# Performance work log

Measured on AMD Instinct MI355X. Metric: run time of the kernel, lower is better.

## Reference

```python
import jax, jax.numpy as jnp
import numpy as np
import math

NB_STEPS = 50          # quadrature sub-intervals -> 51 Clenshaw-Curtis points
NUM_RNN_STEPS = 2


def _cc_weights(nb_steps):
    # Faithful port of UMNN's compute_cc_weights (Clenshaw-Curtis quadrature).
    lam = np.arange(0, nb_steps + 1).reshape(-1, 1).astype(np.float64)
    lam = np.cos((lam @ lam.T) * math.pi / nb_steps)
    lam[:, 0] = 0.5
    lam[:, -1] = 0.5 * lam[:, -1]
    lam = lam * 2.0 / nb_steps
    W = np.arange(0, nb_steps + 1).reshape(-1, 1).astype(np.float64)
    W[np.arange(1, nb_steps + 1, 2)] = 0
    W = 2.0 / (1.0 - W ** 2)
    W[0] = 1.0
    W[np.arange(1, nb_steps + 1, 2)] = 0
    cc = (lam.T @ W).astype(np.float32).reshape(-1)                      # [S]
    steps = np.cos(np.arange(0, nb_steps + 1) * math.pi / nb_steps).astype(np.float32)  # [S]
    return jnp.asarray(cc), jnp.asarray(steps)

CC_W, CC_STEPS = _cc_weights(NB_STEPS)  # S = NB_STEPS + 1 = 51


def _integrand(t, h, W1, b1, W2, b2, W3, b3, final_w):
    # IntegrandNN: MLP(cat(t,h)) -> ELU + 1 (>=0) -> fused power features -> ReLU(Linear)
    z = jnp.concatenate([t, h], axis=1)          # [N, in_d]
    z = jax.nn.relu(z @ W1.T + b1)               # [N, 128]
    z = jax.nn.relu(z @ W2.T + b2)               # [N, 128]
    z = jax.nn.elu(z @ W3.T + b3) + 1.0          # [N, 1], >= 0
    p = jnp.concatenate([z ** 1.5, z ** 2, z ** 2.5, z ** 3, z ** 3.5], axis=1)  # [N, 5]
    return jax.nn.relu((1.0 / (p + 1.0)) @ final_w.T)  # [N, 1]


def _inner_integral(x, h, params):
    # InnerUMNN: integral of IntegrandNN from x to xmax, xmax = max(x) + 10 (global scalar)
    N = x.shape[0]
    S = NB_STEPS + 1
    xmax = jnp.max(x) + 10.0
    T = x + (xmax - x) * (CC_STEPS[None, :] + 1.0) * 0.5   # [N, S]
    Tf = T.reshape(N * S, 1)
    hf = jnp.broadcast_to(h[:, None, :], (N, S, h.shape[1])).reshape(N * S, -1)
    g = _integrand(Tf, hf, *params).reshape(N, S)
    z = jnp.sum(g * CC_W[None, :], axis=1, keepdims=True)  # [N, 1]
    return z * (xmax - x) * 0.5


def _outer_integral(xT, h, params):
    # ParallelNeuralIntegral of InnerUMNN from x0 = 0 to xT; xT: [B, 1]
    B = xT.shape[0]
    S = NB_STEPS + 1
    X = xT * (CC_STEPS[None, :] + 1.0) * 0.5               # [B, S] (x0 = 0)
    Xf = X.reshape(B * S, 1)
    hf = jnp.broadcast_to(h[:, None, :], (B, S, h.shape[1])).reshape(B * S, -1)
    f = _inner_integral(Xf, hf, params).reshape(B, S)      # nested quadrature
    z = jnp.sum(f * CC_W[None, :], axis=1, keepdims=True)  # [B, 1]
    return z * xT * 0.5


def setup_inputs() -> dict:
    key = jax.random.key(0)
    ks = jax.random.split(key, 8)
    B, NF, IN_D, H = 256, 512, 64, 128
    x_ = jax.random.normal(ks[0], (B, NF), jnp.float32)
    h_ = jax.random.normal(ks[1], (B, IN_D - 1), jnp.float32)

    def lin(k, o, i):
        lim = 1.0 / np.sqrt(i)
        kw, kb = jax.random.split(k)
        return (jax.random.uniform(kw, (o, i), jnp.float32, -lim, lim),
                jax.random.uniform(kb, (o,), jnp.float32, -lim, lim))

    W1, b1 = lin(ks[2], H, IN_D)
    W2, b2 = lin(ks[3], H, H)
    W3, b3 = lin(ks[4], 1, H)
    lim5 = 1.0 / np.sqrt(5.0)
    final_w = jnp.abs(jax.random.uniform(ks[5], (1, 5), jnp.float32, -lim5, lim5))  # reset_params: abs
    log_weight = jnp.ones((1, NF), jnp.float32)            # reset_parameters: all ones
    sigmoid_param = jax.random.normal(ks[6], (1,), jnp.float32)
    return dict(x_=x_, h_=h_, W1=W1, b1=b1, W2=W2, b2=b2, W3=W3, b3=b3,
                final_w=final_w, log_weight=log_weight, sigmoid_param=sigmoid_param)


def reference(x_, h_, W1, b1, W2, b2, W3, b3, final_w, log_weight, sigmoid_param):
    params = (W1, b1, W2, b2, W3, b3, final_w)
    # compute_modular_function: F.linear then sum over dim 1 -> [B, 1]
    xm = jnp.sum(x_ @ log_weight.T, axis=1, keepdims=True)
    lam = jax.nn.sigmoid(sigmoid_param)                    # [1]
    out = jnp.zeros_like(xm)
    for _ in range(NUM_RNN_STEPS):
        xT = (1.0 - lam) * xm + lam * out
        out = _outer_integral(xT, h_, params)
    return out
```

## Files before the change

kernel.cpp:

```cpp
#include <hip/hip_runtime.h>
#include <math.h>

#define BB 256
#define NF 512
#define IND 64
#define HD 128
#define SS 51
#define NHM1 63

#define WS_LAM  0
#define WS_CCW  16
#define WS_U    80
#define WS_XM   144
#define WS_OUT1 656
#define WSH_C1  2048
#define WSH_W1  34816
#define WSH_W2F 40960

typedef _Float16 f16x8 __attribute__((ext_vector_type(8)));
typedef float    f32x16 __attribute__((ext_vector_type(16)));

__global__ void k_setup(const float* __restrict__ x_, const float* __restrict__ h_,
                        const float* __restrict__ W1, const float* __restrict__ b1,
                        const float* __restrict__ W2, const float* __restrict__ lw,
                        const float* __restrict__ sp, float* __restrict__ ws) {
    int b = blockIdx.x;
    int j = threadIdx.x;
    short* wsh = (short*)ws;

    float acc = b1[j];
    const float* w1row = W1 + j * IND;
    const float* hrow  = h_ + b * NHM1;
    #pragma unroll 7
    for (int k = 0; k < NHM1; ++k) acc = fmaf(w1row[1 + k], hrow[k], acc);
    {
        _Float16 hv = (_Float16)acc;
        short sv; __builtin_memcpy(&sv, &hv, 2);
        wsh[WSH_C1 + b * HD + j] = sv;
    }

    float s = 0.f;
    for (int k = j; k < NF; k += HD) s = fmaf(x_[b * NF + k], lw[k], s);
    __shared__ float red[HD];
    red[j] = s;
    __syncthreads();
    for (int off = 64; off > 0; off >>= 1) {
        if (j < off) red[j] += red[j + off];
        __syncthreads();
    }
    if (j == 0) ws[WS_XM + b] = red[0];

    if (b < 128) {
        int d = b * 128 + j;
        int i = d & 7, lane = (d >> 3) & 63, kn = d >> 9;
        int kk = kn >> 2, nt = kn & 3;
        int row = nt * 32 + (lane & 31);
        int k = kk * 16 + (lane >> 5) * 8 + i;
        _Float16 hv = (_Float16)W2[row * HD + k];
        short sv; __builtin_memcpy(&sv, &hv, 2);
        wsh[WSH_W2F + d] = sv;
    }

    if (b == 0) {
        if (j < SS) {
            float acc2 = 0.f;
            for (int jj = 0; jj <= 50; jj += 2) {
                float wj = (jj == 0) ? 1.f : 2.f / (1.f - (float)(jj * jj));
                float lamv;
                if (j == 0 || j == 50) {
                    lamv = 0.02f;
                } else {
                    int m = (jj * j) % 100;
                    lamv = cosf((float)m * (float)M_PI / 50.f) * 0.04f;
                }
                acc2 = fmaf(lamv, wj, acc2);
            }
            ws[WS_CCW + j] = acc2;
            float st = cosf((float)j * (float)M_PI / 50.f);
            ws[WS_U + j] = (st + 1.f) * 0.5f;
        }
        if (j == 127) ws[WS_LAM] = 1.f / (1.f + expf(-sp[0]));
    }
    if (b == 2) {
        _Float16 hv = (_Float16)W1[j * IND];
        short sv; __builtin_memcpy(&sv, &hv, 2);
        wsh[WSH_W1 + j] = sv;
    }
    if (b == 4) ws[WS_OUT1 + j] = 0.f;
    if (b == 5) ws[WS_OUT1 + 128 + j] = 0.f;
}

__launch_bounds__(256, 2)
__global__ void k_int(const float* __restrict__ b2, const float* __restrict__ W3,
                      const float* __restrict__ b3, const float* __restrict__ fw,
                      const float* __restrict__ ws, const float* __restrict__ outprev,
                      float* __restrict__ tgt, float* __restrict__ ztgt) {
    int b = blockIdx.x >> 1, half = blockIdx.x & 1;
    int tid = threadIdx.x;
    int wv = tid >> 6, l = tid & 63;
    int e32 = l & 31, h2 = l >> 5;

    __shared__ float us[SS], ccs[SS], xw[4];
    __shared__ float part[2][2][4][32];

    if (ztgt && half == 0 && tid == 0) ztgt[b] = 0.f;
    if (tid < SS) { us[tid] = ws[WS_U + tid]; ccs[tid] = ws[WS_CCW + tid]; }

    float lam = ws[WS_LAM];
    float xmv = ws[WS_XM + tid];
    float opv = outprev ? outprev[tid] : 0.f;
    float xtv = (1.f - lam) * xmv + lam * opv;
    float mx = fmaxf(xtv, 0.f);
    #pragma unroll
    for (int off = 32; off >= 1; off >>= 1) mx = fmaxf(mx, __shfl_xor(mx, off, 64));
    if (l == 0) xw[wv] = mx;
    __syncthreads();
    float xmax = fmaxf(fmaxf(xw[0], xw[1]), fmaxf(xw[2], xw[3])) + 10.f;
    float xT = (1.f - lam) * ws[WS_XM + b] + lam * (outprev ? outprev[b] : 0.f);

    const short* wsh = (const short*)ws;

    f16x8 Af[8], c1r[8], w1r[8];
    #pragma unroll
    for (int kk = 0; kk < 8; ++kk) {
        Af[kk]  = *reinterpret_cast<const f16x8*>(wsh + WSH_W2F + ((kk * 4 + wv) * 64 + l) * 8);
        c1r[kk] = *reinterpret_cast<const f16x8*>(wsh + WSH_C1 + b * HD + kk * 16 + h2 * 8);
        w1r[kk] = *reinterpret_cast<const f16x8*>(wsh + WSH_W1 + kk * 16 + h2 * 8);
    }
    float b2n[16], w3n[16];
    #pragma unroll
    for (int r = 0; r < 16; ++r) {
        int j = wv * 32 + (r & 3) + 8 * (r >> 2) + 4 * h2;
        b2n[r] = b2[j]; w3n[r] = W3[j];
    }
    float b3v = b3[0];
    float fw0 = fw[0], fw1 = fw[1], fw2 = fw[2], fw3 = fw[3], fw4 = fw[4];

    float accO = 0.f;
    int buf = 0;
    int base0 = half * 1344;

    for (int it = 0; it < 21; ++it) {
        int base = base0 + it * 64;
        float t_[2];
        #pragma unroll
        for (int ti = 0; ti < 2; ++ti) {
            int m = base + ti * 32 + e32;
            int mm = m <= 2600 ? m : 2600;
            int s  = (mm * 41121) >> 21;
            int si = mm - s * 51;
            float x = xT * us[s];
            t_[ti] = fmaf(xmax - x, us[si], x);
        }
        _Float16 th0 = (_Float16)t_[0], th1 = (_Float16)t_[1];
        f16x8 tv0 = {th0, th0, th0, th0, th0, th0, th0, th0};
        f16x8 tv1 = {th1, th1, th1, th1, th1, th1, th1, th1};
        f16x8 zf = {};

        f32x16 C0, C1;
        #pragma unroll
        for (int e = 0; e < 16; ++e) { C0[e] = 0.f; C1[e] = 0.f; }

        #pragma unroll
        for (int kk = 0; kk < 8; ++kk) {
            f16x8 B0 = __builtin_elementwise_max(__builtin_elementwise_fma(w1r[kk], tv0, c1r[kk]), zf);
            f16x8 B1 = __builtin_elementwise_max(__builtin_elementwise_fma(w1r[kk], tv1, c1r[kk]), zf);
            C0 = __builtin_amdgcn_mfma_f32_32x32x16_f16(Af[kk], B0, C0, 0, 0, 0);
            C1 = __builtin_amdgcn_mfma_f32_32x32x16_f16(Af[kk], B1, C1, 0, 0, 0);
            __builtin_amdgcn_sched_barrier(0);
        }

        {
            float s0 = 0.f;
            #pragma unroll
            for (int r = 0; r < 16; ++r) s0 = fmaf(fmaxf(C0[r] + b2n[r], 0.f), w3n[r], s0);
            s0 += __shfl_xor(s0, 32, 64);
            if (h2 == 0) part[buf][0][wv][e32] = s0;
            float s1 = 0.f;
            #pragma unroll
            for (int r = 0; r < 16; ++r) s1 = fmaf(fmaxf(C1[r] + b2n[r], 0.f), w3n[r], s1);
            s1 += __shfl_xor(s1, 32, 64);
            if (h2 == 0) part[buf][1][wv][e32] = s1;
        }
        __syncthreads();

        if (wv == 0) {
            int m = base + l;
            float zs = part[buf][h2][0][e32] + part[buf][h2][1][e32]
                     + part[buf][h2][2][e32] + part[buf][h2][3][e32] + b3v;
            float z = zs > 0.f ? zs + 1.f : __expf(zs);
            float sq = sqrtf(z);
            float p15 = z * sq, p2 = z * z, p25 = p2 * sq, p3 = p2 * z, p35 = p3 * sq;
            float g = fw0 * __builtin_amdgcn_rcpf(p15 + 1.f)
                    + fw1 * __builtin_amdgcn_rcpf(p2  + 1.f)
                    + fw2 * __builtin_amdgcn_rcpf(p25 + 1.f)
                    + fw3 * __builtin_amdgcn_rcpf(p3  + 1.f)
                    + fw4 * __builtin_amdgcn_rcpf(p35 + 1.f);
            g = fmaxf(g, 0.f);
            int valid = (m <= 2600);
            int mm = valid ? m : 2600;
            int s  = (mm * 41121) >> 21;
            int si = mm - s * 51;
            float x = xT * us[s];
            float wgt = valid ? (ccs[si] * ccs[s] * (xmax - x) * xT * 0.25f) : 0.f;
            accO = fmaf(g, wgt, accO);
        }
        buf ^= 1;
    }

    if (wv == 0) {
        #pragma unroll
        for (int off = 32; off >= 1; off >>= 1) accO += __shfl_xor(accO, off, 64);
        if (l == 0) atomicAdd(&tgt[b], accO);
    }
}

extern "C" void kernel_launch(void* const* d_in, const int* in_sizes, int n_in,
                              void* d_out, int out_size, void* d_ws, size_t ws_size,
                              hipStream_t stream) {
    (void)in_sizes; (void)n_in; (void)out_size; (void)ws_size;
    const float* x_ = (const float*)d_in[0];
    const float* h_ = (const float*)d_in[1];
    const float* W1 = (const float*)d_in[2];
    const float* b1 = (const float*)d_in[3];
    const float* W2 = (const float*)d_in[4];
    const float* b2 = (const float*)d_in[5];
    const float* W3 = (const float*)d_in[6];
    const float* b3 = (const float*)d_in[7];
    const float* fw = (const float*)d_in[8];
    const float* lw = (const float*)d_in[9];
    const float* sp = (const float*)d_in[10];
    float* wsf  = (float*)d_ws;
    float* out1 = wsf + WS_OUT1;
    float* out  = (float*)d_out;

    k_setup<<<BB, HD, 0, stream>>>(x_, h_, W1, b1, W2, lw, sp, wsf);
    k_int<<<BB * 2, 256, 0, stream>>>(b2, W3, b3, fw, wsf, nullptr, out1, out);
    k_int<<<BB * 2, 256, 0, stream>>>(b2, W3, b3, fw, wsf, out1, out, nullptr);
}
```

Before: 78.55 us.

## Precompute quadrature tables, spread epilogue across waves, defer it one iteration

Each block now builds its quadrature nodes and weights once into shared-memory tables, so the main loop no longer recomputes index decodes. The scalar epilogue (ELU, powers, reciprocals) is split across all four waves at 16 lanes each and delayed by one iteration, so it overlaps the next MFMA batch instead of serialising on wave 0. Smaller changes fold b2 into the accumulator init, split the reduction into four chains, drop the sched_barrier and use packed f16x2 FMAs. The cost is about 10.5 KB more LDS per block and a barrier placed at the end of each iteration.

```diff
diff --git a/kernel.cpp b/kernel.cpp
--- a/kernel.cpp
+++ b/kernel.cpp
@@ -17,8 +17,12 @@
 #define WSH_W1  34816
 #define WSH_W2F 40960
 
+typedef _Float16 f16x2 __attribute__((ext_vector_type(2)));
+typedef _Float16 f16x4 __attribute__((ext_vector_type(4)));
 typedef _Float16 f16x8 __attribute__((ext_vector_type(8)));
 typedef float    f32x16 __attribute__((ext_vector_type(16)));
+
+union f16x8_split { f16x8 v8; f16x2 v2[4]; };
 
 __global__ void k_setup(const float* __restrict__ x_, const float* __restrict__ h_,
                         const float* __restrict__ W1, const float* __restrict__ b1,
@@ -101,6 +105,7 @@
     int e32 = l & 31, h2 = l >> 5;
 
     __shared__ float us[SS], ccs[SS], xw[4];
+    __shared__ float t_tab[1344], wgt_tab[1344];
     __shared__ float part[2][2][4][32];
 
     if (ztgt && half == 0 && tid == 0) ztgt[b] = 0.f;
@@ -118,14 +123,38 @@
     float xmax = fmaxf(fmaxf(xw[0], xw[1]), fmaxf(xw[2], xw[3])) + 10.f;
     float xT = (1.f - lam) * ws[WS_XM + b] + lam * (outprev ? outprev[b] : 0.f);
 
+    int base0 = half * 1344;
+    #pragma unroll
+    for (int k = 0; k < 6; ++k) {
+        int idx = tid + k * 256;
+        if (idx < 1344) {
+            int m = base0 + idx;
+            int valid = (m <= 2600);
+            int mm = valid ? m : 2600;
+            int s  = (mm * 41121) >> 21;
+            int si = mm - s * 51;
+            float x = xT * us[s];
+            float range = xmax - x;
+            t_tab[idx] = fmaf(range, us[si], x);
+            wgt_tab[idx] = valid ? (ccs[si] * ccs[s] * range * xT * 0.25f) : 0.f;
+        }
+    }
+
     const short* wsh = (const short*)ws;
 
-    f16x8 Af[8], c1r[8], w1r[8];
+    f16x8 Af[8];
+    f16x2 c1p[8][4], w1p[8][4];
     #pragma unroll
     for (int kk = 0; kk < 8; ++kk) {
-        Af[kk]  = *reinterpret_cast<const f16x8*>(wsh + WSH_W2F + ((kk * 4 + wv) * 64 + l) * 8);
-        c1r[kk] = *reinterpret_cast<const f16x8*>(wsh + WSH_C1 + b * HD + kk * 16 + h2 * 8);
-        w1r[kk] = *reinterpret_cast<const f16x8*>(wsh + WSH_W1 + kk * 16 + h2 * 8);
+        Af[kk] = *reinterpret_cast<const f16x8*>(wsh + WSH_W2F + ((kk * 4 + wv) * 64 + l) * 8);
+        f16x8_split c8, w8;
+        c8.v8 = *reinterpret_cast<const f16x8*>(wsh + WSH_C1 + b * HD + kk * 16 + h2 * 8);
+        w8.v8 = *reinterpret_cast<const f16x8*>(wsh + WSH_W1 + kk * 16 + h2 * 8);
+        #pragma unroll
+        for (int p = 0; p < 4; ++p) {
+            c1p[kk][p] = c8.v2[p];
+            w1p[kk][p] = w8.v2[p];
+        }
     }
     float b2n[16], w3n[16];
     #pragma unroll
@@ -137,57 +166,71 @@
     float fw0 = fw[0], fw1 = fw[1], fw2 = fw[2], fw3 = fw[3], fw4 = fw[4];
 
     float accO = 0.f;
+    __syncthreads();
+
+    const f16x2 z2 = {(_Float16)0.f, (_Float16)0.f};
     int buf = 0;
-    int base0 = half * 1344;
 
     for (int it = 0; it < 21; ++it) {
-        int base = base0 + it * 64;
-        float t_[2];
-        #pragma unroll
-        for (int ti = 0; ti < 2; ++ti) {
-            int m = base + ti * 32 + e32;
-            int mm = m <= 2600 ? m : 2600;
-            int s  = (mm * 41121) >> 21;
-            int si = mm - s * 51;
-            float x = xT * us[s];
-            t_[ti] = fmaf(xmax - x, us[si], x);
-        }
-        _Float16 th0 = (_Float16)t_[0], th1 = (_Float16)t_[1];
-        f16x8 tv0 = {th0, th0, th0, th0, th0, th0, th0, th0};
-        f16x8 tv1 = {th1, th1, th1, th1, th1, th1, th1, th1};
-        f16x8 zf = {};
+        int base = it * 64;
+        float t0 = t_tab[base + e32];
+        float t1 = t_tab[base + 32 + e32];
+        _Float16 th0 = (_Float16)t0, th1 = (_Float16)t1;
+        f16x2 tv0 = {th0, th0};
+        f16x2 tv1 = {th1, th1};
 
         f32x16 C0, C1;
         #pragma unroll
-        for (int e = 0; e < 16; ++e) { C0[e] = 0.f; C1[e] = 0.f; }
+        for (int e = 0; e < 16; ++e) { C0[e] = b2n[e]; C1[e] = b2n[e]; }
 
         #pragma unroll
         for (int kk = 0; kk < 8; ++kk) {
-            f16x8 B0 = __builtin_elementwise_max(__builtin_elementwise_fma(w1r[kk], tv0, c1r[kk]), zf);
-            f16x8 B1 = __builtin_elementwise_max(__builtin_elementwise_fma(w1r[kk], tv1, c1r[kk]), zf);
-            C0 = __builtin_amdgcn_mfma_f32_32x32x16_f16(Af[kk], B0, C0, 0, 0, 0);
-            C1 = __builtin_amdgcn_mfma_f32_32x32x16_f16(Af[kk], B1, C1, 0, 0, 0);
-            __builtin_amdgcn_sched_barrier(0);
+            f16x8_split B0u, B1u;
+            #pragma unroll
+            for (int p = 0; p < 4; ++p)
+                B0u.v2[p] = __builtin_elementwise_max(
+                    __builtin_elementwise_fma(w1p[kk][p], tv0, c1p[kk][p]), z2);
+            C0 = __builtin_amdgcn_mfma_f32_32x32x16_f16(Af[kk], B0u.v8, C0, 0, 0, 0);
+            #pragma unroll
+            for (int p = 0; p < 4; ++p)
+                B1u.v2[p] = __builtin_elementwise_max(
+                    __builtin_elementwise_fma(w1p[kk][p], tv1, c1p[kk][p]), z2);
+            C1 = __builtin_amdgcn_mfma_f32_32x32x16_f16(Af[kk], B1u.v8, C1, 0, 0, 0);
         }
 
         {
-            float s0 = 0.f;
-            #pragma unroll
-            for (int r = 0; r < 16; ++r) s0 = fmaf(fmaxf(C0[r] + b2n[r], 0.f), w3n[r], s0);
+            float sa = 0.f, sb = 0.f, sc = 0.f, sd = 0.f;
+            #pragma unroll
+            for (int r = 0; r < 4; ++r) {
+                sa = fmaf(fmaxf(C0[r],      0.f), w3n[r],      sa);
+                sb = fmaf(fmaxf(C0[r + 4],  0.f), w3n[r + 4],  sb);
+                sc = fmaf(fmaxf(C0[r + 8],  0.f), w3n[r + 8],  sc);
+                sd = fmaf(fmaxf(C0[r + 12], 0.f), w3n[r + 12], sd);
+            }
+            float s0 = (sa + sb) + (sc + sd);
             s0 += __shfl_xor(s0, 32, 64);
             if (h2 == 0) part[buf][0][wv][e32] = s0;
-            float s1 = 0.f;
-            #pragma unroll
-            for (int r = 0; r < 16; ++r) s1 = fmaf(fmaxf(C1[r] + b2n[r], 0.f), w3n[r], s1);
+
+            sa = sb = sc = sd = 0.f;
+            #pragma unroll
+            for (int r = 0; r < 4; ++r) {
+                sa = fmaf(fmaxf(C1[r],      0.f), w3n[r],      sa);
+                sb = fmaf(fmaxf(C1[r + 4],  0.f), w3n[r + 4],  sb);
+                sc = fmaf(fmaxf(C1[r + 8],  0.f), w3n[r + 8],  sc);
+                sd = fmaf(fmaxf(C1[r + 12], 0.f), w3n[r + 12], sd);
+            }
+            float s1 = (sa + sb) + (sc + sd);
             s1 += __shfl_xor(s1, 32, 64);
             if (h2 == 0) part[buf][1][wv][e32] = s1;
         }
-        __syncthreads();
-
-        if (wv == 0) {
-            int m = base + l;
-            float zs = part[buf][h2][0][e32] + part[buf][h2][1][e32]
-                     + part[buf][h2][2][e32] + part[buf][h2][3][e32] + b3v;
+
+        if (it > 0 && l < 16) {
+            int pbuf = buf ^ 1;
+            int pbase = base - 64;
+            int e_loc = wv * 16 + l;
+            int ti = e_loc >> 5, ec = e_loc & 31;
+            float zs = part[pbuf][ti][0][ec] + part[pbuf][ti][1][ec]
+                     + part[pbuf][ti][2][ec] + part[pbuf][ti][3][ec] + b3v;
             float z = zs > 0.f ? zs + 1.f : __expf(zs);
             float sq = sqrtf(z);
             float p15 = z * sq, p2 = z * z, p25 = p2 * sq, p3 = p2 * z, p35 = p3 * sq;
@@ -197,22 +240,34 @@
                     + fw3 * __builtin_amdgcn_rcpf(p3  + 1.f)
                     + fw4 * __builtin_amdgcn_rcpf(p35 + 1.f);
             g = fmaxf(g, 0.f);
-            int valid = (m <= 2600);
-            int mm = valid ? m : 2600;
-            int s  = (mm * 41121) >> 21;
-            int si = mm - s * 51;
-            float x = xT * us[s];
-            float wgt = valid ? (ccs[si] * ccs[s] * (xmax - x) * xT * 0.25f) : 0.f;
-            accO = fmaf(g, wgt, accO);
-        }
+            accO = fmaf(g, wgt_tab[pbase + e_loc], accO);
+        }
+        __syncthreads();
         buf ^= 1;
     }
 
-    if (wv == 0) {
-        #pragma unroll
-        for (int off = 32; off >= 1; off >>= 1) accO += __shfl_xor(accO, off, 64);
-        if (l == 0) atomicAdd(&tgt[b], accO);
-    }
+    if (l < 16) {
+        int pbuf = buf ^ 1;
+        int pbase = 20 * 64;
+        int e_loc = wv * 16 + l;
+        int ti = e_loc >> 5, ec = e_loc & 31;
+        float zs = part[pbuf][ti][0][ec] + part[pbuf][ti][1][ec]
+                 + part[pbuf][ti][2][ec] + part[pbuf][ti][3][ec] + b3v;
+        float z = zs > 0.f ? zs + 1.f : __expf(zs);
+        float sq = sqrtf(z);
+        float p15 = z * sq, p2 = z * z, p25 = p2 * sq, p3 = p2 * z, p35 = p3 * sq;
+        float g = fw0 * __builtin_amdgcn_rcpf(p15 + 1.f)
+                + fw1 * __builtin_amdgcn_rcpf(p2  + 1.f)
+                + fw2 * __builtin_amdgcn_rcpf(p25 + 1.f)
+                + fw3 * __builtin_amdgcn_rcpf(p3  + 1.f)
+                + fw4 * __builtin_amdgcn_rcpf(p35 + 1.f);
+        g = fmaxf(g, 0.f);
+        accO = fmaf(g, wgt_tab[pbase + e_loc], accO);
+    }
+
+    #pragma unroll
+    for (int off = 8; off >= 1; off >>= 1) accO += __shfl_xor(accO, off, 64);
+    if (l == 0) atomicAdd(&tgt[b], accO);
 }
 
 extern "C" void kernel_launch(void* const* d_in, const int* in_sizes, int n_in,
```

Result: slower. 85.05 us (+8.3%).

## Give each wave all 128 output rows and drop cross-wave LDS reduction

Applied to the files above, without the earlier changes.

Each wave now computes all four 32-row tiles of the second layer for its own 32 points, holding all of W2 in registers. This removes the shared-memory partial-sum exchange and the per-iteration __syncthreads. It also launches one block per batch row instead of two, initialises the accumulators with b2, and overlaps the scalar tail math of the previous iteration with the current MFMAs. In exchange, register pressure rises sharply (launch bounds drop to 1 block per CU), the grid halves, and the packed f16x2 FMAs may not lower as cleanly.

```diff
diff --git a/kernel.cpp b/kernel.cpp
--- a/kernel.cpp
+++ b/kernel.cpp
@@ -17,8 +17,11 @@
 #define WSH_W1  34816
 #define WSH_W2F 40960
 
+typedef _Float16 f16x2 __attribute__((ext_vector_type(2)));
 typedef _Float16 f16x8 __attribute__((ext_vector_type(8)));
 typedef float    f32x16 __attribute__((ext_vector_type(16)));
+
+union f16x8_split { f16x8 v8; f16x2 v2[4]; };
 
 __global__ void k_setup(const float* __restrict__ x_, const float* __restrict__ h_,
                         const float* __restrict__ W1, const float* __restrict__ b1,
@@ -90,20 +93,19 @@
     if (b == 5) ws[WS_OUT1 + 128 + j] = 0.f;
 }
 
-__launch_bounds__(256, 2)
+__launch_bounds__(256, 1)
 __global__ void k_int(const float* __restrict__ b2, const float* __restrict__ W3,
                       const float* __restrict__ b3, const float* __restrict__ fw,
                       const float* __restrict__ ws, const float* __restrict__ outprev,
                       float* __restrict__ tgt, float* __restrict__ ztgt) {
-    int b = blockIdx.x >> 1, half = blockIdx.x & 1;
+    int b = blockIdx.x;
     int tid = threadIdx.x;
     int wv = tid >> 6, l = tid & 63;
     int e32 = l & 31, h2 = l >> 5;
 
     __shared__ float us[SS], ccs[SS], xw[4];
-    __shared__ float part[2][2][4][32];
-
-    if (ztgt && half == 0 && tid == 0) ztgt[b] = 0.f;
+
+    if (ztgt && tid == 0) ztgt[b] = 0.f;
     if (tid < SS) { us[tid] = ws[WS_U + tid]; ccs[tid] = ws[WS_CCW + tid]; }
 
     float lam = ws[WS_LAM];
@@ -120,75 +122,62 @@
 
     const short* wsh = (const short*)ws;
 
-    f16x8 Af[8], c1r[8], w1r[8];
+    f16x8 Af[8][4];
+    #pragma unroll
+    for (int kk = 0; kk < 8; ++kk)
+        #pragma unroll
+        for (int nt = 0; nt < 4; ++nt)
+            Af[kk][nt] = *reinterpret_cast<const f16x8*>(
+                wsh + WSH_W2F + ((kk * 4 + nt) * 64 + l) * 8);
+
+    f16x2 c1p[8][4], w1p[8][4];
     #pragma unroll
     for (int kk = 0; kk < 8; ++kk) {
-        Af[kk]  = *reinterpret_cast<const f16x8*>(wsh + WSH_W2F + ((kk * 4 + wv) * 64 + l) * 8);
-        c1r[kk] = *reinterpret_cast<const f16x8*>(wsh + WSH_C1 + b * HD + kk * 16 + h2 * 8);
-        w1r[kk] = *reinterpret_cast<const f16x8*>(wsh + WSH_W1 + kk * 16 + h2 * 8);
-    }
-    float b2n[16], w3n[16];
-    #pragma unroll
-    for (int r = 0; r < 16; ++r) {
-        int j = wv * 32 + (r & 3) + 8 * (r >> 2) + 4 * h2;
-        b2n[r] = b2[j]; w3n[r] = W3[j];
-    }
+        f16x8_split c8, w8;
+        c8.v8 = *reinterpret_cast<const f16x8*>(wsh + WSH_C1 + b * HD + kk * 16 + h2 * 8);
+        w8.v8 = *reinterpret_cast<const f16x8*>(wsh + WSH_W1 + kk * 16 + h2 * 8);
+        #pragma unroll
+        for (int p = 0; p < 4; ++p) { c1p[kk][p] = c8.v2[p]; w1p[kk][p] = w8.v2[p]; }
+    }
+
+    float b2n[4][16], w3n[4][16];
+    #pragma unroll
+    for (int nt = 0; nt < 4; ++nt)
+        #pragma unroll
+        for (int r = 0; r < 16; ++r) {
+            int j = nt * 32 + (r & 3) + 8 * (r >> 2) + 4 * h2;
+            b2n[nt][r] = b2[j]; w3n[nt][r] = W3[j];
+        }
     float b3v = b3[0];
     float fw0 = fw[0], fw1 = fw[1], fw2 = fw[2], fw3 = fw[3], fw4 = fw[4];
 
     float accO = 0.f;
-    int buf = 0;
-    int base0 = half * 1344;
-
+    float zs_prev = 0.f, w_prev = 0.f;
+
+    #pragma unroll 1
     for (int it = 0; it < 21; ++it) {
-        int base = base0 + it * 64;
-        float t_[2];
-        #pragma unroll
-        for (int ti = 0; ti < 2; ++ti) {
-            int m = base + ti * 32 + e32;
-            int mm = m <= 2600 ? m : 2600;
-            int s  = (mm * 41121) >> 21;
-            int si = mm - s * 51;
-            float x = xT * us[s];
-            t_[ti] = fmaf(xmax - x, us[si], x);
-        }
-        _Float16 th0 = (_Float16)t_[0], th1 = (_Float16)t_[1];
-        f16x8 tv0 = {th0, th0, th0, th0, th0, th0, th0, th0};
-        f16x8 tv1 = {th1, th1, th1, th1, th1, th1, th1, th1};
-        f16x8 zf = {};
-
-        f32x16 C0, C1;
-        #pragma unroll
-        for (int e = 0; e < 16; ++e) { C0[e] = 0.f; C1[e] = 0.f; }
-
-        #pragma unroll
-        for (int kk = 0; kk < 8; ++kk) {
-            f16x8 B0 = __builtin_elementwise_max(__builtin_elementwise_fma(w1r[kk], tv0, c1r[kk]), zf);
-            f16x8 B1 = __builtin_elementwise_max(__builtin_elementwise_fma(w1r[kk], tv1, c1r[kk]), zf);
-            C0 = __builtin_amdgcn_mfma_f32_32x32x16_f16(Af[kk], B0, C0, 0, 0, 0);
-            C1 = __builtin_amdgcn_mfma_f32_32x32x16_f16(Af[kk], B1, C1, 0, 0, 0);
-            __builtin_amdgcn_sched_barrier(0);
+        int m = (wv * 21 + it) * 32 + e32;
+        int valid = (m <= 2600);
+        int mm = valid ? m : 2600;
+        int s  = (mm * 41121) >> 21;
+        int si = mm - s * 51;
+        float x = xT * us[s];
+        float range = xmax - x;
+        float t = fmaf(range, us[si], x);
+        float wgt = valid ? (ccs[si] * ccs[s] * range * xT * 0.25f) : 0.f;
+        float wsel = h2 ? 0.f : wgt;
+        _Float16 th = (_Float16)t;
+        f16x2 tv = {th, th};
+
+        f32x16 C0, C1, C2, C3;
+        #pragma unroll
+        for (int e = 0; e < 16; ++e) {
+            C0[e] = b2n[0][e]; C1[e] = b2n[1][e];
+            C2[e] = b2n[2][e]; C3[e] = b2n[3][e];
         }
 
         {
-            float s0 = 0.f;
-            #pragma unroll
-            for (int r = 0; r < 16; ++r) s0 = fmaf(fmaxf(C0[r] + b2n[r], 0.f), w3n[r], s0);
-            s0 += __shfl_xor(s0, 32, 64);
-            if (h2 == 0) part[buf][0][wv][e32] = s0;
-            float s1 = 0.f;
-            #pragma unroll
-            for (int r = 0; r < 16; ++r) s1 = fmaf(fmaxf(C1[r] + b2n[r], 0.f), w3n[r], s1);
-            s1 += __shfl_xor(s1, 32, 64);
-            if (h2 == 0) part[buf][1][wv][e32] = s1;
-        }
-        __syncthreads();
-
-        if (wv == 0) {
-            int m = base + l;
-            float zs = part[buf][h2][0][e32] + part[buf][h2][1][e32]
-                     + part[buf][h2][2][e32] + part[buf][h2][3][e32] + b3v;
-            float z = zs > 0.f ? zs + 1.f : __expf(zs);
+            float z = zs_prev > 0.f ? zs_prev + 1.f : __expf(zs_prev);
             float sq = sqrtf(z);
             float p15 = z * sq, p2 = z * z, p25 = p2 * sq, p3 = p2 * z, p35 = p3 * sq;
             float g = fw0 * __builtin_amdgcn_rcpf(p15 + 1.f)
@@ -197,22 +186,53 @@
                     + fw3 * __builtin_amdgcn_rcpf(p3  + 1.f)
                     + fw4 * __builtin_amdgcn_rcpf(p35 + 1.f);
             g = fmaxf(g, 0.f);
-            int valid = (m <= 2600);
-            int mm = valid ? m : 2600;
-            int s  = (mm * 41121) >> 21;
-            int si = mm - s * 51;
-            float x = xT * us[s];
-            float wgt = valid ? (ccs[si] * ccs[s] * (xmax - x) * xT * 0.25f) : 0.f;
-            accO = fmaf(g, wgt, accO);
-        }
-        buf ^= 1;
-    }
-
-    if (wv == 0) {
-        #pragma unroll
-        for (int off = 32; off >= 1; off >>= 1) accO += __shfl_xor(accO, off, 64);
-        if (l == 0) atomicAdd(&tgt[b], accO);
-    }
+            accO = fmaf(g, w_prev, accO);
+        }
+
+        const f16x2 z2 = {(_Float16)0.f, (_Float16)0.f};
+        #pragma unroll
+        for (int kk = 0; kk < 8; ++kk) {
+            f16x8_split Bu;
+            #pragma unroll
+            for (int p = 0; p < 4; ++p)
+                Bu.v2[p] = __builtin_elementwise_max(
+                    __builtin_elementwise_fma(w1p[kk][p], tv, c1p[kk][p]), z2);
+            C0 = __builtin_amdgcn_mfma_f32_32x32x16_f16(Af[kk][0], Bu.v8, C0, 0, 0, 0);
+            C1 = __builtin_amdgcn_mfma_f32_32x32x16_f16(Af[kk][1], Bu.v8, C1, 0, 0, 0);
+            C2 = __builtin_amdgcn_mfma_f32_32x32x16_f16(Af[kk][2], Bu.v8, C2, 0, 0, 0);
+            C3 = __builtin_amdgcn_mfma_f32_32x32x16_f16(Af[kk][3], Bu.v8, C3, 0, 0, 0);
+        }
+
+        float pa = 0.f, pb = 0.f, pc = 0.f, pd = 0.f;
+        #pragma unroll
+        for (int r = 0; r < 16; ++r) {
+            pa = fmaf(fmaxf(C0[r], 0.f), w3n[0][r], pa);
+            pb = fmaf(fmaxf(C1[r], 0.f), w3n[1][r], pb);
+            pc = fmaf(fmaxf(C2[r], 0.f), w3n[2][r], pc);
+            pd = fmaf(fmaxf(C3[r], 0.f), w3n[3][r], pd);
+        }
+        float z1 = (pa + pb) + (pc + pd);
+        z1 += __shfl_xor(z1, 32, 64);
+        zs_prev = z1 + b3v;
+        w_prev = wsel;
+    }
+
+    {
+        float z = zs_prev > 0.f ? zs_prev + 1.f : __expf(zs_prev);
+        float sq = sqrtf(z);
+        float p15 = z * sq, p2 = z * z, p25 = p2 * sq, p3 = p2 * z, p35 = p3 * sq;
+        float g = fw0 * __builtin_amdgcn_rcpf(p15 + 1.f)
+                + fw1 * __builtin_amdgcn_rcpf(p2  + 1.f)
+                + fw2 * __builtin_amdgcn_rcpf(p25 + 1.f)
+                + fw3 * __builtin_amdgcn_rcpf(p3  + 1.f)
+                + fw4 * __builtin_amdgcn_rcpf(p35 + 1.f);
+        g = fmaxf(g, 0.f);
+        accO = fmaf(g, w_prev, accO);
+    }
+
+    #pragma unroll
+    for (int off = 32; off >= 1; off >>= 1) accO += __shfl_xor(accO, off, 64);
+    if (l == 0) atomicAdd(&tgt[b], accO);
 }
 
 extern "C" void kernel_launch(void* const* d_in, const int* in_sizes, int n_in,
@@ -235,6 +255,6 @@
     float* out  = (float*)d_out;
 
     k_setup<<<BB, HD, 0, stream>>>(x_, h_, W1, b1, W2, lw, sp, wsf);
-    k_int<<<BB * 2, 256, 0, stream>>>(b2, W3, b3, fw, wsf, nullptr, out1, out);
-    k_int<<<BB * 2, 256, 0, stream>>>(b2, W3, b3, fw, wsf, out1, out, nullptr);
+    k_int<<<BB, 256, 0, stream>>>(b2, W3, b3, fw, wsf, nullptr, out1, out);
+    k_int<<<BB, 256, 0, stream>>>(b2, W3, b3, fw, wsf, out1, out, nullptr);
 }
```

New measurement: 73.16 us, median of 2. 1.07x faster.
